# Kernel optimization log

Hardware: AMD Instinct MI355X
Metric: run time of the kernel (lower is better)

The kernel has to match this reference:

```python
import jax, jax.numpy as jnp
import numpy as np
from jax import lax

BN_EPS = 1e-5

def _tern(w):
    # TWN-style ternarization with straight-through estimator
    d = 0.7 * jnp.mean(jnp.abs(w))
    q = jnp.where(jnp.abs(w) > d, jnp.sign(w), jnp.zeros_like(w))
    return w + lax.stop_gradient(q - w)

def _conv(x, w, b):
    y = lax.conv_general_dilated(x, _tern(w), (1, 1), 'SAME',
                                 dimension_numbers=('NCHW', 'OIHW', 'NCHW'))
    return y + b[None, :, None, None]

def _bn4(x, g, b, m, v):
    inv = g * lax.rsqrt(v + BN_EPS)
    return (x - m[None, :, None, None]) * inv[None, :, None, None] + b[None, :, None, None]

def _bn2(x, g, b, m, v):
    return (x - m) * (g * lax.rsqrt(v + BN_EPS)) + b

def _pool(x):
    return lax.reduce_window(x, -jnp.inf, lax.max, (1, 1, 2, 2), (1, 1, 2, 2), 'VALID')


def setup_inputs() -> dict:
    key = jax.random.key(0)
    ks = jax.random.split(key, 8)
    f = jnp.float32
    d = {}
    d['x'] = jax.random.normal(ks[0], (1024, 1, 28, 28), f)
    wshapes = {'w1': (32, 1, 3, 3), 'w2': (64, 32, 3, 3), 'w3': (128, 64, 3, 3),
               'w4': (128, 128, 3, 3), 'wf1': (256, 6272), 'wf2': (128, 256), 'wf3': (10, 128)}
    for i, (n, s) in enumerate(wshapes.items()):
        d[n] = jax.random.normal(ks[i + 1], s, f) * 0.1
    for n, c in [('1', 32), ('2', 64), ('3', 128), ('4', 128)]:
        d['b' + n] = jnp.zeros((c,), f)
        d['g' + n] = jnp.ones((c,), f)
        d['be' + n] = jnp.zeros((c,), f)
        d['m' + n] = jnp.zeros((c,), f)
        d['v' + n] = jnp.ones((c,), f)
    for n, c in [('f1', 256), ('f2', 128)]:
        d['b' + n] = jnp.zeros((c,), f)
        d['g' + n] = jnp.ones((c,), f)
        d['be' + n] = jnp.zeros((c,), f)
        d['m' + n] = jnp.zeros((c,), f)
        d['v' + n] = jnp.ones((c,), f)
    d['bf3'] = jnp.zeros((10,), f)
    return d


def reference(x, w1, b1, g1, be1, m1, v1, w2, b2, g2, be2, m2, v2,
              w3, b3, g3, be3, m3, v3, w4, b4, g4, be4, m4, v4,
              wf1, bf1, gf1, bef1, mf1, vf1, wf2, bf2, gf2, bef2, mf2, vf2,
              wf3, bf3):
    h = jax.nn.relu(_bn4(_conv(x, w1, b1), g1, be1, m1, v1))
    h = jax.nn.relu(_bn4(_conv(h, w2, b2), g2, be2, m2, v2))
    h = _pool(h)                                  # [B,64,14,14]
    h = jax.nn.relu(_bn4(_conv(h, w3, b3), g3, be3, m3, v3))
    h = jax.nn.relu(_bn4(_conv(h, w4, b4), g4, be4, m4, v4))
    h = _pool(h)                                  # [B,128,7,7]
    h = h.reshape(h.shape[0], -1)                 # [B,6272]
    h = jax.nn.relu(_bn2(h @ _tern(wf1).T + bf1, gf1, bef1, mf1, vf1))
    h = jax.nn.relu(_bn2(h @ _tern(wf2).T + bf2, gf2, bef2, mf2, vf2))
    return h @ _tern(wf3).T + bf3                 # [B,10] logits
```

## Files before the change

### kernel.cpp

```cpp
#include <hip/hip_runtime.h>
#include <hip/hip_bf16.h>

#define BN_EPS 1e-5f

typedef __attribute__((ext_vector_type(8))) short bf16x8;
typedef __attribute__((ext_vector_type(4))) float f32x4;
typedef unsigned short u16;
typedef unsigned int u32;

__device__ __forceinline__ void load16(const void* g, void* l) {
    __builtin_amdgcn_global_load_lds((const __attribute__((address_space(1))) void*)g,
                                     (__attribute__((address_space(3))) void*)l, 16, 0, 0);
}
__device__ __forceinline__ u16 f2b(float v) {
    __hip_bfloat16 h = __float2bfloat16(v);
    return *reinterpret_cast<u16*>(&h);
}
__device__ __forceinline__ float ternq(float x, float d) {
    return (fabsf(x) > d) ? (x > 0.f ? 1.f : -1.f) : 0.f;
}

constexpr size_t ALGN(size_t x) { return (x + 255) & ~(size_t)255; }
constexpr size_t O_SUMS = 0;
constexpr size_t O_W1R  = 256;
constexpr size_t O_WF2Q = ALGN(O_W1R + 288 * 4);
constexpr size_t O_WF3Q = ALGN(O_WF2Q + 32768 * 4);
constexpr size_t O_BQ2  = ALGN(O_WF3Q + 1280 * 4);
constexpr size_t O_BQ3  = ALGN(O_BQ2 + 64 * 288 * 2);
constexpr size_t O_BQ4  = ALGN(O_BQ3 + 128 * 576 * 2);
constexpr size_t O_BQF1 = ALGN(O_BQ4 + 128 * 1152 * 2);
constexpr size_t O_F1   = ALGN(O_BQF1 + (size_t)256 * 6272 * 2);
constexpr size_t O_F2   = ALGN(O_F1 + 1024 * 256 * 4);
constexpr size_t O_ACT1 = ALGN(O_F2 + 1024 * 128 * 4);
constexpr size_t O_ACT2 = ALGN(O_ACT1 + (size_t)1024 * 900 * 32 * 2);
constexpr size_t O_ACT3 = ALGN(O_ACT2 + (size_t)1024 * 256 * 64 * 2);
constexpr size_t O_ACT4 = ALGN(O_ACT3 + (size_t)1024 * 256 * 128 * 2);

__global__ void zero_sums(float* s) { if (threadIdx.x < 8) s[threadIdx.x] = 0.f; }

__device__ void absmean_seg(const float* __restrict__ w, int n4, float* __restrict__ sum,
                            int b0, int nb) {
    __shared__ float sm[256];
    float s = 0.f;
    for (int i = b0 * 256 + threadIdx.x; i < n4; i += nb * 256) {
        float4 v = ((const float4*)w)[i];
        s += fabsf(v.x) + fabsf(v.y) + fabsf(v.z) + fabsf(v.w);
    }
    sm[threadIdx.x] = s;
    __syncthreads();
    for (int o = 128; o > 0; o >>= 1) {
        if (threadIdx.x < o) sm[threadIdx.x] += sm[threadIdx.x + o];
        __syncthreads();
    }
    if (threadIdx.x == 0) atomicAdd(sum, sm[0]);
}

__global__ void absmean_all(const float* w1, const float* w2, const float* w3, const float* w4,
                            const float* wf1, const float* wf2, const float* wf3, float* sums) {
    int b = blockIdx.x;
    if (b < 160)      absmean_seg(wf1, 401408, sums + 4, b, 160);
    else if (b < 192) absmean_seg(w4, 36864, sums + 3, b - 160, 32);
    else if (b < 208) absmean_seg(w3, 18432, sums + 2, b - 192, 16);
    else if (b < 216) absmean_seg(w2, 4608, sums + 1, b - 208, 8);
    else if (b < 224) absmean_seg(wf2, 8192, sums + 5, b - 216, 8);
    else if (b < 225) absmean_seg(w1, 72, sums + 0, 0, 1);
    else              absmean_seg(wf3, 320, sums + 6, 0, 1);
}

__device__ void tern_conv_seg(const float* __restrict__ w, float d, u16* __restrict__ bq,
                              int COUT, int CIN, int b0, int nb) {
    int N = COUT * CIN * 9;
    for (int i = b0 * 256 + threadIdx.x; i < N; i += nb * 256) {
        float q = ternq(w[i], d);
        int co = i / (CIN * 9), r = i % (CIN * 9);
        int ci = r / 9, tap = r % 9;
        bq[(size_t)co * CIN * 9 + tap * CIN + ci] = f2b(q);
    }
}
__device__ void tern_conv_prime_seg(const float* __restrict__ w, float d, u16* __restrict__ bqp,
                                    int CIN, int b0, int nb) {
    int N = 128 * CIN * 9;
    for (int i = b0 * 256 + threadIdx.x; i < N; i += nb * 256) {
        float q = ternq(w[i], d);
        int co = i / (CIN * 9), r = i % (CIN * 9);
        int ci = r / 9, tap = r % 9;
        int k = tap * CIN + ci;
        int s = k >> 5, qd = (k & 31) >> 3, e = k & 7;
        int lane = qd * 16 + (co & 15), nt = co >> 4;
        bqp[((size_t)(s * 8 + nt) * 64 + lane) * 8 + e] = f2b(q);
    }
}
__device__ void tern_f32_seg(const float* __restrict__ w, float d, float* __restrict__ wq,
                             int N, int b0, int nb) {
    for (int i = b0 * 256 + threadIdx.x; i < N; i += nb * 256) wq[i] = ternq(w[i], d);
}

__global__ void tern_all(const float* w1, const float* w2, const float* w3, const float* w4,
                         const float* wf1, const float* wf2, const float* wf3,
                         const float* __restrict__ sums,
                         float* w1r, u16* bq2, u16* bq3p, u16* bq4p, u16* bqf1,
                         float* wf2q, float* wf3q) {
    int b = blockIdx.x;
    if (b < 1) {
        tern_f32_seg(w1, 0.7f * sums[0] / 288.f, w1r, 288, 0, 1);
    } else if (b < 9) {
        tern_conv_seg(w2, 0.7f * sums[1] / 18432.f, bq2, 64, 32, b - 1, 8);
    } else if (b < 41) {
        tern_conv_prime_seg(w3, 0.7f * sums[2] / 73728.f, bq3p, 64, b - 9, 32);
    } else if (b < 105) {
        tern_conv_prime_seg(w4, 0.7f * sums[3] / 147456.f, bq4p, 128, b - 41, 64);
    } else if (b < 617) {
        float d = 0.7f * sums[4] / 1605632.f;
        for (int i = (b - 105) * 256 + threadIdx.x; i < 1605632; i += 512 * 256) {
            float q = ternq(wf1[i], d);
            int j = i / 6272, k = i % 6272;
            int c = k / 49, s = k % 49;
            bqf1[(size_t)j * 6272 + s * 128 + c] = f2b(q);
        }
    } else if (b < 633) {
        tern_f32_seg(wf2, 0.7f * sums[5] / 32768.f, wf2q, 32768, b - 617, 16);
    } else {
        tern_f32_seg(wf3, 0.7f * sums[6] / 1280.f, wf3q, 1280, 0, 1);
    }
}

__global__ void zero_f1(float* f1) {
    ((float4*)f1)[blockIdx.x * 256 + threadIdx.x] = make_float4(0.f, 0.f, 0.f, 0.f);
}

__global__ __launch_bounds__(256)
void conv1_direct(const float* __restrict__ x, const float* __restrict__ w1r,
                  const float* __restrict__ bias, const float* __restrict__ gam,
                  const float* __restrict__ bet, const float* __restrict__ mu,
                  const float* __restrict__ var, u16* __restrict__ out) {
    __shared__ float xs[784];
    __shared__ float wsh[288];
    __shared__ float scl[32], sft[32];
    const int n = blockIdx.x, tid = threadIdx.x;
    for (int i = tid; i < 784; i += 256) xs[i] = x[(size_t)n * 784 + i];
    for (int i = tid; i < 288; i += 256) wsh[i] = w1r[i];
    if (tid < 32) {
        float s = gam[tid] * rsqrtf(var[tid] + BN_EPS);
        scl[tid] = s;
        sft[tid] = (bias[tid] - mu[tid]) * s + bet[tid];
    }
    __syncthreads();
    for (int p = tid; p < 784; p += 256) {
        int y = p / 28, xx = p % 28;
        float patch[9];
#pragma unroll
        for (int dy = 0; dy < 3; ++dy)
#pragma unroll
            for (int dx = 0; dx < 3; ++dx) {
                int gy = y + dy - 1, gx = xx + dx - 1;
                patch[dy * 3 + dx] = (gy >= 0 && gy < 28 && gx >= 0 && gx < 28) ? xs[gy * 28 + gx] : 0.f;
            }
        u32 pk[16];
#pragma unroll
        for (int co = 0; co < 32; co += 2) {
            float s0 = 0.f, s1 = 0.f;
#pragma unroll
            for (int t = 0; t < 9; ++t) {
                s0 += wsh[co * 9 + t] * patch[t];
                s1 += wsh[(co + 1) * 9 + t] * patch[t];
            }
            float v0 = fmaxf(s0 * scl[co] + sft[co], 0.f);
            float v1 = fmaxf(s1 * scl[co + 1] + sft[co + 1], 0.f);
            pk[co >> 1] = ((u32)f2b(v1) << 16) | (u32)f2b(v0);
        }
        size_t base = ((size_t)(n * 30 + y + 1) * 30 + (xx + 1)) * 32;
#pragma unroll
        for (int q = 0; q < 4; ++q) ((uint4*)(out + base))[q] = ((uint4*)pk)[q];
    }
}

template<int C, int HP, int HV>
__global__ void border_zero(u16* __restrict__ buf) {
    constexpr int NB = 2 * HP + 2 * HV;
    constexpr int CG = C / 8;
    int i = blockIdx.x * blockDim.x + threadIdx.x;
    if (i >= 1024 * NB * CG) return;
    int cg = i % CG, r = i / CG;
    int b = r % NB, n = r / NB;
    int py, px;
    if (b < HP)               { py = 0;                  px = b; }
    else if (b < 2 * HP)      { py = HP - 1;             px = b - HP; }
    else if (b < 2 * HP + HV) { py = b - 2 * HP + 1;     px = 0; }
    else                      { py = b - 2 * HP - HV + 1; px = HP - 1; }
    size_t off = ((size_t)(n * HP + py) * HP + px) * C + cg * 8;
    *(uint4*)(buf + off) = make_uint4(0, 0, 0, 0);
}

template<int CIN, int BN, int HV, int HP, int G, bool POOL, bool PADOUT>
__global__ __launch_bounds__(256)
void convgemm(const u16* __restrict__ act, const u16* __restrict__ bq,
              const float* __restrict__ bias, const float* __restrict__ gam,
              const float* __restrict__ bet, const float* __restrict__ mu,
              const float* __restrict__ var, u16* __restrict__ out) {
    constexpr int BM = 128;
    constexpr int K = 9 * CIN;
    constexpr int S = K / (32 * G);
    constexpr int TPC = CIN / 32;
    constexpr int NT = BN / 32;
    constexpr int RB = BN / 64;
    constexpr int HO = HV / 2;
    constexpr int PP = POOL ? HO * HO : HV * HV;

    __shared__ __align__(16) u16 Alds[G][BM * 32];
    __shared__ __align__(16) u16 Blds[G][BN * 32];
    __shared__ int rowA[BM];
    __shared__ int rowO[BM];
    __shared__ float scl[BN], sft[BN];

    const int tid = threadIdx.x;
    const int m0 = blockIdx.x * BM;

    for (int t = tid; t < BM; t += 256) {
        int base;
        if (POOL) {
            int p = (m0 >> 2) + (t >> 2), q = t & 3;
            int n = p / PP, rr = p % PP;
            int oy = rr / HO, ox = rr % HO;
            int y = oy * 2 + (q >> 1), x = ox * 2 + (q & 1);
            base = ((n * HP + y) * HP + x) * CIN;
        } else {
            int m = m0 + t;
            int n = m / PP, rr = m % PP;
            int y = rr / HV, x = rr % HV;
            base = ((n * HP + y) * HP + x) * CIN;
        }
        rowA[t] = base;
    }
    if (POOL) {
        if (tid < 32) {
            int p = (m0 >> 2) + tid;
            int n = p / PP, rr = p % PP;
            int oy = rr / HO, ox = rr % HO;
            rowO[tid] = PADOUT ? ((n * 16 + oy + 1) * 16 + ox + 1) * BN : p * BN;
        }
    } else {
        for (int t = tid; t < BM; t += 256) {
            int m = m0 + t;
            int n = m / PP, rr = m % PP;
            int y = rr / HV, x = rr % HV;
            rowO[t] = PADOUT ? ((n * 16 + y + 1) * 16 + x + 1) * BN : m * BN;
        }
    }
    if (tid < BN) {
        float s = gam[tid] * rsqrtf(var[tid] + BN_EPS);
        scl[tid] = s;
        sft[tid] = (bias[tid] - mu[tid]) * s + bet[tid];
    }
    __syncthreads();

    int arow[2];
    arow[0] = rowA[(tid >> 6) * 16 + (tid & 15)];
    arow[1] = rowA[64 + (tid >> 6) * 16 + (tid & 15)];
    const int chunkb = ((tid >> 4) & 3) * 16;
    const int bco = (tid >> 6) * 16 + (tid & 15);
    const char* actb = (const char*)act;
    const char* bqb  = (const char*)bq;

    const int wave = tid >> 6, lane = tid & 63;
    const int wm = wave & 1, wn = wave >> 1;
    const int fr16 = lane * 16;

    f32x4 acc[4][NT] = {};

    for (int s = 0; s < S; ++s) {
#pragma unroll
        for (int j = 0; j < G; ++j) {
            int g = s * G + j;
            int tap = g / TPC, cio = (g % TPC) * 32;
            int dy = tap / 3, dx = tap % 3;
            int toffb = ((dy * HP + dx) * CIN + cio) * 2;
            char* Al = (char*)Alds[j];
#pragma unroll
            for (int r = 0; r < 2; ++r)
                load16(actb + (size_t)arow[r] * 2 + toffb + chunkb, Al + r * 4096 + tid * 16);
            char* Bl = (char*)Blds[j];
            int bkob = g * 64 + chunkb;
#pragma unroll
            for (int r = 0; r < RB; ++r)
                load16(bqb + (size_t)(r * 64 + bco) * K * 2 + bkob, Bl + r * 4096 + tid * 16);
        }
        __syncthreads();
#pragma unroll
        for (int j = 0; j < G; ++j) {
            const char* Al = (const char*)Alds[j];
            const char* Bl = (const char*)Blds[j];
            bf16x8 af[4], bf[NT];
#pragma unroll
            for (int mt = 0; mt < 4; ++mt)
                af[mt] = *(const bf16x8*)(Al + (wm * 4 + mt) * 1024 + fr16);
#pragma unroll
            for (int nt = 0; nt < NT; ++nt)
                bf[nt] = *(const bf16x8*)(Bl + (wn * NT + nt) * 1024 + fr16);
#pragma unroll
            for (int mt = 0; mt < 4; ++mt)
#pragma unroll
                for (int nt = 0; nt < NT; ++nt)
                    acc[mt][nt] = __builtin_amdgcn_mfma_f32_16x16x32_bf16(af[mt], bf[nt], acc[mt][nt], 0, 0, 0);
        }
        __syncthreads();
    }

    const int fr = lane & 15, quad = lane >> 4;
    if (POOL) {
#pragma unroll
        for (int mt = 0; mt < 4; ++mt) {
            int pl = wm * 16 + mt * 4 + quad;
            int ob = rowO[pl];
#pragma unroll
            for (int nt = 0; nt < NT; ++nt) {
                int col = wn * (NT * 16) + nt * 16 + fr;
                float sc = scl[col], sh = sft[col];
                f32x4 a = acc[mt][nt];
                float v0 = a[0] * sc + sh, v1 = a[1] * sc + sh;
                float v2 = a[2] * sc + sh, v3 = a[3] * sc + sh;
                float mx = fmaxf(fmaxf(v0, v1), fmaxf(v2, v3));
                out[(size_t)ob + col] = f2b(fmaxf(mx, 0.f));
            }
        }
    } else {
#pragma unroll
        for (int mt = 0; mt < 4; ++mt) {
            int rb = wm * 64 + mt * 16 + quad * 4;
            int o0 = rowO[rb], o1 = rowO[rb + 1], o2 = rowO[rb + 2], o3 = rowO[rb + 3];
#pragma unroll
            for (int nt = 0; nt < NT; ++nt) {
                int col = wn * (NT * 16) + nt * 16 + fr;
                float sc = scl[col], sh = sft[col];
                f32x4 a = acc[mt][nt];
                out[(size_t)o0 + col] = f2b(fmaxf(a[0] * sc + sh, 0.f));
                out[(size_t)o1 + col] = f2b(fmaxf(a[1] * sc + sh, 0.f));
                out[(size_t)o2 + col] = f2b(fmaxf(a[2] * sc + sh, 0.f));
                out[(size_t)o3 + col] = f2b(fmaxf(a[3] * sc + sh, 0.f));
            }
        }
    }
}

__global__ __launch_bounds__(256)
void conv34(const u16* __restrict__ act2p, const u16* __restrict__ b3p, const u16* __restrict__ b4p,
            const float* __restrict__ b3, const float* __restrict__ g3, const float* __restrict__ be3,
            const float* __restrict__ m3, const float* __restrict__ v3,
            const float* __restrict__ b4, const float* __restrict__ g4, const float* __restrict__ be4,
            const float* __restrict__ m4, const float* __restrict__ v4,
            u16* __restrict__ out) {
    __shared__ __align__(16) char X[290 * 272];

    const int tid = threadIdx.x;
    const int n = blockIdx.x;
    const int w = tid >> 6, lane = tid & 63;
    const int fr = lane & 15, quad = lane >> 4;

    {
        const uint4* src = (const uint4*)(act2p + (size_t)n * 16384);
#pragma unroll
        for (int it = 0; it < 8; ++it) {
            int i = it * 256 + tid;
            int r = i >> 3, c = i & 7;
            *(uint4*)(X + (r + 17) * 144 + c * 16) = src[i];
        }
    }
    __syncthreads();

    const int mb = w * 64 + fr;
    f32x4 acc[4][8] = {};

    {
        const char* B3 = (const char*)b3p;
        int ab[4];
#pragma unroll
        for (int mt = 0; mt < 4; ++mt) ab[mt] = (mb + mt * 16) * 144 + quad * 16;
#pragma unroll 1
        for (int tap = 0; tap < 9; ++tap) {
            const int ib = ((tap / 3) * 16 + (tap % 3)) * 144;
#pragma unroll
            for (int h = 0; h < 2; ++h) {
                const int s = tap * 2 + h;
                bf16x8 af[4], bf[8];
#pragma unroll
                for (int mt = 0; mt < 4; ++mt)
                    af[mt] = *(const bf16x8*)(X + ab[mt] + ib + h * 64);
#pragma unroll
                for (int nt = 0; nt < 8; ++nt)
                    bf[nt] = *(const bf16x8*)(B3 + (size_t)((s * 8 + nt) * 64 + lane) * 16);
#pragma unroll
                for (int mt = 0; mt < 4; ++mt)
#pragma unroll
                    for (int nt = 0; nt < 8; ++nt)
                        acc[mt][nt] = __builtin_amdgcn_mfma_f32_16x16x32_bf16(af[mt], bf[nt], acc[mt][nt], 0, 0, 0);
            }
        }
    }
    __syncthreads();

    {
        float scl3[8], sft3[8];
#pragma unroll
        for (int nt = 0; nt < 8; ++nt) {
            int c = nt * 16 + fr;
            float s = g3[c] * rsqrtf(v3[c] + BN_EPS);
            scl3[nt] = s;
            sft3[nt] = (b3[c] - m3[c]) * s + be3[c];
        }
        for (int t = tid; t < 960; t += 256) {
            int ch = t & 15, b = t >> 4;
            int m = (b < 16) ? b : (b < 32) ? 224 + b : (b < 46) ? (b - 31) * 16 : (b - 45) * 16 + 15;
            *(uint4*)(X + (m + 17) * 272 + ch * 16) = make_uint4(0, 0, 0, 0);
        }
#pragma unroll
        for (int mt = 0; mt < 4; ++mt) {
            int y = w * 4 + mt;
            if (y >= 1 && y <= 14) {
#pragma unroll
                for (int j = 0; j < 4; ++j) {
                    int x = quad * 4 + j;
                    if (x >= 1 && x <= 14) {
                        char* row = X + (y * 16 + x + 17) * 272;
#pragma unroll
                        for (int nt = 0; nt < 8; ++nt) {
                            int col = nt * 16 + fr;
                            float v = fmaxf(acc[mt][nt][j] * scl3[nt] + sft3[nt], 0.f);
                            *(u16*)(row + col * 2) = f2b(v);
                        }
                    }
                }
            }
        }
    }
    __syncthreads();

#pragma unroll
    for (int a = 0; a < 4; ++a)
#pragma unroll
        for (int b = 0; b < 8; ++b) acc[a][b] = (f32x4){0.f, 0.f, 0.f, 0.f};
    {
        const char* B4 = (const char*)b4p;
        int ab[4];
#pragma unroll
        for (int mt = 0; mt < 4; ++mt) ab[mt] = (mb + mt * 16) * 272 + quad * 16;
#pragma unroll 1
        for (int tap = 0; tap < 9; ++tap) {
            const int ib = ((tap / 3) * 16 + (tap % 3)) * 272;
#pragma unroll
            for (int qr = 0; qr < 4; ++qr) {
                const int s = tap * 4 + qr;
                bf16x8 af[4], bf[8];
#pragma unroll
                for (int mt = 0; mt < 4; ++mt)
                    af[mt] = *(const bf16x8*)(X + ab[mt] + ib + qr * 64);
#pragma unroll
                for (int nt = 0; nt < 8; ++nt)
                    bf[nt] = *(const bf16x8*)(B4 + (size_t)((s * 8 + nt) * 64 + lane) * 16);
#pragma unroll
                for (int mt = 0; mt < 4; ++mt)
#pragma unroll
                    for (int nt = 0; nt < 8; ++nt)
                        acc[mt][nt] = __builtin_amdgcn_mfma_f32_16x16x32_bf16(af[mt], bf[nt], acc[mt][nt], 0, 0, 0);
            }
        }
    }
    __syncthreads();

    {
        float scl4[8], sft4[8];
#pragma unroll
        for (int nt = 0; nt < 8; ++nt) {
            int c = nt * 16 + fr;
            float s = g4[c] * rsqrtf(v4[c] + BN_EPS);
            scl4[nt] = s;
            sft4[nt] = (b4[c] - m4[c]) * s + be4[c];
        }
#pragma unroll
        for (int mt = 0; mt < 4; ++mt) {
#pragma unroll
            for (int j = 0; j < 4; ++j) {
                char* row = X + (w * 64 + mt * 16 + quad * 4 + j + 17) * 272;
#pragma unroll
                for (int nt = 0; nt < 8; ++nt) {
                    int col = nt * 16 + fr;
                    float v = fmaxf(acc[mt][nt][j] * scl4[nt] + sft4[nt], 0.f);
                    *(u16*)(row + col * 2) = f2b(v);
                }
            }
        }
    }
    __syncthreads();

    for (int t = tid; t < 784; t += 256) {
        int ch = t & 15, p = t >> 4;
        int oy = p / 7, ox = p % 7;
        int r00 = (2 * oy + 1) * 16 + (2 * ox + 1) + 17;
        uint4 A0 = *(const uint4*)(X + (r00) * 272 + ch * 16);
        uint4 A1 = *(const uint4*)(X + (r00 + 1) * 272 + ch * 16);
        uint4 A2 = *(const uint4*)(X + (r00 + 16) * 272 + ch * 16);
        uint4 A3 = *(const uint4*)(X + (r00 + 17) * 272 + ch * 16);
        const u16* pa = (const u16*)&A0;
        const u16* pb = (const u16*)&A1;
        const u16* pc = (const u16*)&A2;
        const u16* pd = (const u16*)&A3;
        u16 o[8];
#pragma unroll
        for (int e = 0; e < 8; ++e)
            o[e] = (u16)max(max((int)pa[e], (int)pb[e]), max((int)pc[e], (int)pd[e]));
        *(uint4*)(out + ((size_t)n * 49 + p) * 128 + ch * 8) = *(const uint4*)o;
    }
}

__global__ __launch_bounds__(256)
void fc1gemm(const u16* __restrict__ A, const u16* __restrict__ Bq, float* __restrict__ out) {
    constexpr int K = 6272, KC = 896, S = KC / 64;
    __shared__ __align__(16) u16 Alds[2][128 * 32];
    __shared__ __align__(16) u16 Blds[2][128 * 32];
    const int tid = threadIdx.x;
    const int m0 = blockIdx.x * 128;
    const int n0 = blockIdx.y * 128;
    const int k0 = blockIdx.z * KC;
    const int chunkb = ((tid >> 4) & 3) * 16;
    const int rr = (tid >> 6) * 16 + (tid & 15);
    const char* Ag = (const char*)A;
    const char* Bg = (const char*)Bq;
    const int wave = tid >> 6, lane = tid & 63;
    const int wm = wave & 1, wn = wave >> 1;
    const int fr16 = lane * 16;
    f32x4 acc[4][4] = {};

    for (int s = 0; s < S; ++s) {
#pragma unroll
        for (int j = 0; j < 2; ++j) {
            int kb = (k0 + s * 64 + j * 32) * 2 + chunkb;
            char* Al = (char*)Alds[j];
            char* Bl = (char*)Blds[j];
#pragma unroll
            for (int r = 0; r < 2; ++r) {
                load16(Ag + (size_t)(m0 + r * 64 + rr) * K * 2 + kb, Al + r * 4096 + tid * 16);
                load16(Bg + (size_t)(n0 + r * 64 + rr) * K * 2 + kb, Bl + r * 4096 + tid * 16);
            }
        }
        __syncthreads();
#pragma unroll
        for (int j = 0; j < 2; ++j) {
            const char* Al = (const char*)Alds[j];
            const char* Bl = (const char*)Blds[j];
            bf16x8 af[4], bf[4];
#pragma unroll
            for (int mt = 0; mt < 4; ++mt)
                af[mt] = *(const bf16x8*)(Al + (wm * 4 + mt) * 1024 + fr16);
#pragma unroll
            for (int nt = 0; nt < 4; ++nt)
                bf[nt] = *(const bf16x8*)(Bl + (wn * 4 + nt) * 1024 + fr16);
#pragma unroll
            for (int mt = 0; mt < 4; ++mt)
#pragma unroll
                for (int nt = 0; nt < 4; ++nt)
                    acc[mt][nt] = __builtin_amdgcn_mfma_f32_16x16x32_bf16(af[mt], bf[nt], acc[mt][nt], 0, 0, 0);
        }
        __syncthreads();
    }
    const int fr = lane & 15, quad = lane >> 4;
#pragma unroll
    for (int mt = 0; mt < 4; ++mt) {
        int row = m0 + wm * 64 + mt * 16 + quad * 4;
#pragma unroll
        for (int nt = 0; nt < 4; ++nt) {
            int col = n0 + wn * 64 + nt * 16 + fr;
            f32x4 a = acc[mt][nt];
            atomicAdd(&out[(size_t)(row + 0) * 256 + col], a[0]);
            atomicAdd(&out[(size_t)(row + 1) * 256 + col], a[1]);
            atomicAdd(&out[(size_t)(row + 2) * 256 + col], a[2]);
            atomicAdd(&out[(size_t)(row + 3) * 256 + col], a[3]);
        }
    }
}

__global__ __launch_bounds__(256)
void fc2_kernel(const float* __restrict__ A, const float* __restrict__ Bw,
                const float* __restrict__ bA, const float* __restrict__ gA,
                const float* __restrict__ beA, const float* __restrict__ mA,
                const float* __restrict__ vA,
                const float* __restrict__ bias, const float* __restrict__ gam,
                const float* __restrict__ bet, const float* __restrict__ mu,
                const float* __restrict__ var, float* __restrict__ out) {
    constexpr int Nn = 128, K = 256;
    __shared__ __align__(16) float As[16][68];
    __shared__ __align__(16) float Bs[16][68];
    __shared__ float sclA[256], sftA[256];
    const int tid = threadIdx.x;
    const int n0 = blockIdx.x * 64, m0 = blockIdx.y * 64;
    if (tid < 256) {
        float s = gA[tid] * rsqrtf(vA[tid] + BN_EPS);
        sclA[tid] = s;
        sftA[tid] = (bA[tid] - mA[tid]) * s + beA[tid];
    }
    const int tm = tid >> 4, tn = tid & 15;
    const int lr = tid >> 2, lk = (tid & 3) * 4;
    float acc[4][4] = {};
    __syncthreads();
    for (int k0 = 0; k0 < K; k0 += 16) {
        float4 av = *(const float4*)&A[(size_t)(m0 + lr) * K + k0 + lk];
        float4 bv = *(const float4*)&Bw[(size_t)(n0 + lr) * K + k0 + lk];
        As[lk + 0][lr] = fmaxf(av.x * sclA[k0 + lk + 0] + sftA[k0 + lk + 0], 0.f);
        As[lk + 1][lr] = fmaxf(av.y * sclA[k0 + lk + 1] + sftA[k0 + lk + 1], 0.f);
        As[lk + 2][lr] = fmaxf(av.z * sclA[k0 + lk + 2] + sftA[k0 + lk + 2], 0.f);
        As[lk + 3][lr] = fmaxf(av.w * sclA[k0 + lk + 3] + sftA[k0 + lk + 3], 0.f);
        Bs[lk + 0][lr] = bv.x; Bs[lk + 1][lr] = bv.y; Bs[lk + 2][lr] = bv.z; Bs[lk + 3][lr] = bv.w;
        __syncthreads();
#pragma unroll
        for (int k = 0; k < 16; ++k) {
            float4 a = *(const float4*)&As[k][tm * 4];
            float4 b = *(const float4*)&Bs[k][tn * 4];
            acc[0][0] += a.x * b.x; acc[0][1] += a.x * b.y; acc[0][2] += a.x * b.z; acc[0][3] += a.x * b.w;
            acc[1][0] += a.y * b.x; acc[1][1] += a.y * b.y; acc[1][2] += a.y * b.z; acc[1][3] += a.y * b.w;
            acc[2][0] += a.z * b.x; acc[2][1] += a.z * b.y; acc[2][2] += a.z * b.z; acc[2][3] += a.z * b.w;
            acc[3][0] += a.w * b.x; acc[3][1] += a.w * b.y; acc[3][2] += a.w * b.z; acc[3][3] += a.w * b.w;
        }
        __syncthreads();
    }
#pragma unroll
    for (int i = 0; i < 4; ++i) {
        int row = m0 + tm * 4 + i;
#pragma unroll
        for (int j = 0; j < 4; ++j) {
            int col = n0 + tn * 4 + j;
            float sc = gam[col] * rsqrtf(var[col] + BN_EPS);
            float v = (acc[i][j] + bias[col] - mu[col]) * sc + bet[col];
            out[(size_t)row * Nn + col] = fmaxf(v, 0.f);
        }
    }
}

__global__ __launch_bounds__(256)
void fc3_kernel(const float* __restrict__ A, const float* __restrict__ Bw,
                const float* __restrict__ bias, float* __restrict__ out) {
    int i = blockIdx.x * blockDim.x + threadIdx.x;
    if (i >= 1024 * 10) return;
    int n = i / 10, j = i % 10;
    const float4* a = (const float4*)&A[(size_t)n * 128];
    const float4* b = (const float4*)&Bw[(size_t)j * 128];
    float s = 0.f;
#pragma unroll
    for (int k = 0; k < 32; ++k) {
        float4 x = a[k], y = b[k];
        s += x.x * y.x + x.y * y.y + x.z * y.z + x.w * y.w;
    }
    out[i] = s + bias[j];
}

extern "C" void kernel_launch(void* const* d_in, const int* in_sizes, int n_in,
                              void* d_out, int out_size, void* d_ws, size_t ws_size,
                              hipStream_t stream) {
    (void)in_sizes; (void)n_in; (void)out_size; (void)ws_size;
    const float* x   = (const float*)d_in[0];
    const float* w1  = (const float*)d_in[1];
    const float* w2  = (const float*)d_in[2];
    const float* w3  = (const float*)d_in[3];
    const float* w4  = (const float*)d_in[4];
    const float* wf1 = (const float*)d_in[5];
    const float* wf2 = (const float*)d_in[6];
    const float* wf3 = (const float*)d_in[7];
    auto P = [&](int i) { return (const float*)d_in[i]; };
    char* wsb = (char*)d_ws;
    float* sums = (float*)(wsb + O_SUMS);
    float* w1r  = (float*)(wsb + O_W1R);
    float* wf2q = (float*)(wsb + O_WF2Q);
    float* wf3q = (float*)(wsb + O_WF3Q);
    u16* bq2   = (u16*)(wsb + O_BQ2);
    u16* bq3p  = (u16*)(wsb + O_BQ3);
    u16* bq4p  = (u16*)(wsb + O_BQ4);
    u16* bqf1  = (u16*)(wsb + O_BQF1);
    float* f1  = (float*)(wsb + O_F1);
    float* f2  = (float*)(wsb + O_F2);
    u16* act1  = (u16*)(wsb + O_ACT1);
    u16* act2p = (u16*)(wsb + O_ACT2);
    u16* act4p = (u16*)(wsb + O_ACT4);

    zero_sums<<<1, 64, 0, stream>>>(sums);
    absmean_all<<<226, 256, 0, stream>>>(w1, w2, w3, w4, wf1, wf2, wf3, sums);
    tern_all<<<634, 256, 0, stream>>>(w1, w2, w3, w4, wf1, wf2, wf3, sums,
                                      w1r, bq2, bq3p, bq4p, bqf1, wf2q, wf3q);

    border_zero<32, 30, 28><<<(1024 * 116 * 4 + 255) / 256, 256, 0, stream>>>(act1);
    border_zero<64, 16, 14><<<(1024 * 60 * 8 + 255) / 256, 256, 0, stream>>>(act2p);
    zero_f1<<<256, 256, 0, stream>>>(f1);

    conv1_direct<<<1024, 256, 0, stream>>>(x, w1r, P(8), P(9), P(10), P(11), P(12), act1);
    convgemm<32, 64, 28, 30, 1, true, true><<<6272, 256, 0, stream>>>(
        act1, bq2, P(13), P(14), P(15), P(16), P(17), act2p);
    conv34<<<1024, 256, 0, stream>>>(
        act2p, bq3p, bq4p,
        P(18), P(19), P(20), P(21), P(22),
        P(23), P(24), P(25), P(26), P(27), act4p);
    fc1gemm<<<dim3(8, 2, 7), 256, 0, stream>>>(act4p, bqf1, f1);
    fc2_kernel<<<dim3(2, 16), 256, 0, stream>>>(
        f1, wf2q, P(28), P(29), P(30), P(31), P(32),
        P(33), P(34), P(35), P(36), P(37), f2);
    fc3_kernel<<<40, 256, 0, stream>>>(f2, wf3q, P(38), (float*)d_out);
}
```

Before: 432.8 us.

## Skip padding rows in conv34 and retile waves as 2x2 over M and N

The fused conv3/conv4 kernel now computes only the 14 interior row-tiles of the padded 16x16 grid instead of all 16. Each wave handles 7 row tiles by 64 output channels in a 2x2 wave grid, rather than 4 row tiles by 128 channels. The shared buffer drops the extra top halo rows, which cuts LDS from 290 to 258 rows. This removes MFMA work spent on border rows that were discarded, and changes the register footprint (28 accumulators instead of 32) and the A/B fragment reuse ratio.

```diff
diff --git a/kernel.cpp b/kernel.cpp
--- a/kernel.cpp
+++ b/kernel.cpp
@@ -348,11 +348,12 @@
             const float* __restrict__ b4, const float* __restrict__ g4, const float* __restrict__ be4,
             const float* __restrict__ m4, const float* __restrict__ v4,
             u16* __restrict__ out) {
-    __shared__ __align__(16) char X[290 * 272];
+    __shared__ __align__(16) char X[258 * 272];
 
     const int tid = threadIdx.x;
     const int n = blockIdx.x;
-    const int w = tid >> 6, lane = tid & 63;
+    const int wave = tid >> 6, lane = tid & 63;
+    const int wm = wave & 1, wn = wave >> 1;
     const int fr = lane & 15, quad = lane >> 4;
 
     {
@@ -361,47 +362,47 @@
         for (int it = 0; it < 8; ++it) {
             int i = it * 256 + tid;
             int r = i >> 3, c = i & 7;
-            *(uint4*)(X + (r + 17) * 144 + c * 16) = src[i];
-        }
-    }
-    __syncthreads();
-
-    const int mb = w * 64 + fr;
-    f32x4 acc[4][8] = {};
+            *(uint4*)(X + (r + 1) * 144 + c * 16) = src[i];
+        }
+    }
+    __syncthreads();
+
+    f32x4 acc[7][4] = {};
 
     {
         const char* B3 = (const char*)b3p;
-        int ab[4];
-#pragma unroll
-        for (int mt = 0; mt < 4; ++mt) ab[mt] = (mb + mt * 16) * 144 + quad * 16;
+        int ab[7];
+#pragma unroll
+        for (int mtl = 0; mtl < 7; ++mtl)
+            ab[mtl] = ((wm * 7 + mtl + 1) * 16 + fr) * 144 + quad * 16;
 #pragma unroll 1
         for (int tap = 0; tap < 9; ++tap) {
-            const int ib = ((tap / 3) * 16 + (tap % 3)) * 144;
+            const int ib = ((tap / 3) * 16 + (tap % 3) - 16) * 144;
 #pragma unroll
             for (int h = 0; h < 2; ++h) {
                 const int s = tap * 2 + h;
-                bf16x8 af[4], bf[8];
-#pragma unroll
-                for (int mt = 0; mt < 4; ++mt)
-                    af[mt] = *(const bf16x8*)(X + ab[mt] + ib + h * 64);
-#pragma unroll
-                for (int nt = 0; nt < 8; ++nt)
-                    bf[nt] = *(const bf16x8*)(B3 + (size_t)((s * 8 + nt) * 64 + lane) * 16);
-#pragma unroll
-                for (int mt = 0; mt < 4; ++mt)
-#pragma unroll
-                    for (int nt = 0; nt < 8; ++nt)
-                        acc[mt][nt] = __builtin_amdgcn_mfma_f32_16x16x32_bf16(af[mt], bf[nt], acc[mt][nt], 0, 0, 0);
+                bf16x8 af[7], bf[4];
+#pragma unroll
+                for (int mtl = 0; mtl < 7; ++mtl)
+                    af[mtl] = *(const bf16x8*)(X + ab[mtl] + ib + h * 64);
+#pragma unroll
+                for (int nt = 0; nt < 4; ++nt)
+                    bf[nt] = *(const bf16x8*)(B3 + (size_t)((s * 8 + wn * 4 + nt) * 64 + lane) * 16);
+#pragma unroll
+                for (int mtl = 0; mtl < 7; ++mtl)
+#pragma unroll
+                    for (int nt = 0; nt < 4; ++nt)
+                        acc[mtl][nt] = __builtin_amdgcn_mfma_f32_16x16x32_bf16(af[mtl], bf[nt], acc[mtl][nt], 0, 0, 0);
             }
         }
     }
     __syncthreads();
 
     {
-        float scl3[8], sft3[8];
-#pragma unroll
-        for (int nt = 0; nt < 8; ++nt) {
-            int c = nt * 16 + fr;
+        float scl3[4], sft3[4];
+#pragma unroll
+        for (int nt = 0; nt < 4; ++nt) {
+            int c = wn * 64 + nt * 16 + fr;
             float s = g3[c] * rsqrtf(v3[c] + BN_EPS);
             scl3[nt] = s;
             sft3[nt] = (b3[c] - m3[c]) * s + be3[c];
@@ -409,23 +410,21 @@
         for (int t = tid; t < 960; t += 256) {
             int ch = t & 15, b = t >> 4;
             int m = (b < 16) ? b : (b < 32) ? 224 + b : (b < 46) ? (b - 31) * 16 : (b - 45) * 16 + 15;
-            *(uint4*)(X + (m + 17) * 272 + ch * 16) = make_uint4(0, 0, 0, 0);
-        }
-#pragma unroll
-        for (int mt = 0; mt < 4; ++mt) {
-            int y = w * 4 + mt;
-            if (y >= 1 && y <= 14) {
-#pragma unroll
-                for (int j = 0; j < 4; ++j) {
-                    int x = quad * 4 + j;
-                    if (x >= 1 && x <= 14) {
-                        char* row = X + (y * 16 + x + 17) * 272;
-#pragma unroll
-                        for (int nt = 0; nt < 8; ++nt) {
-                            int col = nt * 16 + fr;
-                            float v = fmaxf(acc[mt][nt][j] * scl3[nt] + sft3[nt], 0.f);
-                            *(u16*)(row + col * 2) = f2b(v);
-                        }
+            *(uint4*)(X + (m + 1) * 272 + ch * 16) = make_uint4(0, 0, 0, 0);
+        }
+#pragma unroll
+        for (int mtl = 0; mtl < 7; ++mtl) {
+            int y = wm * 7 + mtl + 1;
+#pragma unroll
+            for (int j = 0; j < 4; ++j) {
+                int x = quad * 4 + j;
+                if (x >= 1 && x <= 14) {
+                    char* row = X + (y * 16 + x + 1) * 272;
+#pragma unroll
+                    for (int nt = 0; nt < 4; ++nt) {
+                        int col = wn * 64 + nt * 16 + fr;
+                        float v = fmaxf(acc[mtl][nt][j] * scl3[nt] + sft3[nt], 0.f);
+                        *(u16*)(row + col * 2) = f2b(v);
                     }
                 }
             }
@@ -434,55 +433,57 @@
     __syncthreads();
 
 #pragma unroll
-    for (int a = 0; a < 4; ++a)
-#pragma unroll
-        for (int b = 0; b < 8; ++b) acc[a][b] = (f32x4){0.f, 0.f, 0.f, 0.f};
+    for (int a = 0; a < 7; ++a)
+#pragma unroll
+        for (int b = 0; b < 4; ++b) acc[a][b] = (f32x4){0.f, 0.f, 0.f, 0.f};
     {
         const char* B4 = (const char*)b4p;
-        int ab[4];
-#pragma unroll
-        for (int mt = 0; mt < 4; ++mt) ab[mt] = (mb + mt * 16) * 272 + quad * 16;
+        int ab[7];
+#pragma unroll
+        for (int mtl = 0; mtl < 7; ++mtl)
+            ab[mtl] = ((wm * 7 + mtl + 1) * 16 + fr) * 272 + quad * 16;
 #pragma unroll 1
         for (int tap = 0; tap < 9; ++tap) {
-            const int ib = ((tap / 3) * 16 + (tap % 3)) * 272;
+            const int ib = ((tap / 3) * 16 + (tap % 3) - 16) * 272;
 #pragma unroll
             for (int qr = 0; qr < 4; ++qr) {
                 const int s = tap * 4 + qr;
-                bf16x8 af[4], bf[8];
-#pragma unroll
-                for (int mt = 0; mt < 4; ++mt)
-                    af[mt] = *(const bf16x8*)(X + ab[mt] + ib + qr * 64);
-#pragma unroll
-                for (int nt = 0; nt < 8; ++nt)
-                    bf[nt] = *(const bf16x8*)(B4 + (size_t)((s * 8 + nt) * 64 + lane) * 16);
-#pragma unroll
-                for (int mt = 0; mt < 4; ++mt)
-#pragma unroll
-                    for (int nt = 0; nt < 8; ++nt)
-                        acc[mt][nt] = __builtin_amdgcn_mfma_f32_16x16x32_bf16(af[mt], bf[nt], acc[mt][nt], 0, 0, 0);
+                bf16x8 af[7], bf[4];
+#pragma unroll
+                for (int mtl = 0; mtl < 7; ++mtl)
+                    af[mtl] = *(const bf16x8*)(X + ab[mtl] + ib + qr * 64);
+#pragma unroll
+                for (int nt = 0; nt < 4; ++nt)
+                    bf[nt] = *(const bf16x8*)(B4 + (size_t)((s * 8 + wn * 4 + nt) * 64 + lane) * 16);
+#pragma unroll
+                for (int mtl = 0; mtl < 7; ++mtl)
+#pragma unroll
+                    for (int nt = 0; nt < 4; ++nt)
+                        acc[mtl][nt] = __builtin_amdgcn_mfma_f32_16x16x32_bf16(af[mtl], bf[nt], acc[mtl][nt], 0, 0, 0);
             }
         }
     }
     __syncthreads();
 
     {
-        float scl4[8], sft4[8];
-#pragma unroll
-        for (int nt = 0; nt < 8; ++nt) {
-            int c = nt * 16 + fr;
+        float scl4[4], sft4[4];
+#pragma unroll
+        for (int nt = 0; nt < 4; ++nt) {
+            int c = wn * 64 + nt * 16 + fr;
             float s = g4[c] * rsqrtf(v4[c] + BN_EPS);
             scl4[nt] = s;
             sft4[nt] = (b4[c] - m4[c]) * s + be4[c];
         }
 #pragma unroll
-        for (int mt = 0; mt < 4; ++mt) {
+        for (int mtl = 0; mtl < 7; ++mtl) {
+            int y = wm * 7 + mtl + 1;
 #pragma unroll
             for (int j = 0; j < 4; ++j) {
-                char* row = X + (w * 64 + mt * 16 + quad * 4 + j + 17) * 272;
-#pragma unroll
-                for (int nt = 0; nt < 8; ++nt) {
-                    int col = nt * 16 + fr;
-                    float v = fmaxf(acc[mt][nt][j] * scl4[nt] + sft4[nt], 0.f);
+                char* row = X + (y * 16 + quad * 4 + j + 1) * 272;
+#pragma unroll
+                for (int nt = 0; nt < 4; ++nt) {
+                    int col = wn * 64 + nt * 16 + fr;
+                    float v = fmaxf(acc[mtl][nt][j] * scl4[nt] + sft4[nt], 0.f);
                     *(u16*)(row + col * 2) = f2b(v);
                 }
             }
@@ -493,7 +494,7 @@
     for (int t = tid; t < 784; t += 256) {
         int ch = t & 15, p = t >> 4;
         int oy = p / 7, ox = p % 7;
-        int r00 = (2 * oy + 1) * 16 + (2 * ox + 1) + 17;
+        int r00 = (2 * oy + 1) * 16 + (2 * ox + 1) + 1;
         uint4 A0 = *(const uint4*)(X + (r00) * 272 + ch * 16);
         uint4 A1 = *(const uint4*)(X + (r00 + 1) * 272 + ch * 16);
         uint4 A2 = *(const uint4*)(X + (r00 + 16) * 272 + ch * 16);
```

Result: faster. 418.5 us (-3.3%).
